# Kernel optimization log

Measured on AMD Instinct MI355X. Metric: run time of the kernel, lower is better.

Reference implementation:

```python
import jax, jax.numpy as jnp
import numpy as np

INPUT, HIDDEN, OUTPUT = 512, 1024, 512

def setup_inputs() -> dict:
    key = jax.random.key(0)
    ks = jax.random.split(key, 7)
    s_in = 1.0 / np.sqrt(INPUT)
    s_h = 1.0 / np.sqrt(HIDDEN)
    return {
        "x": jax.random.normal(ks[0], (64, 512, INPUT), dtype=jnp.float32),
        "W_in": jax.random.uniform(ks[1], (INPUT, HIDDEN), minval=-s_in, maxval=s_in, dtype=jnp.float32),
        "b_in": jax.random.uniform(ks[2], (HIDDEN,), minval=-s_in, maxval=s_in, dtype=jnp.float32),
        "W_h": jax.random.uniform(ks[3], (HIDDEN, HIDDEN), minval=-s_h, maxval=s_h, dtype=jnp.float32),
        "b_h": jax.random.uniform(ks[4], (HIDDEN,), minval=-s_h, maxval=s_h, dtype=jnp.float32),
        "W_out": jax.random.uniform(ks[5], (HIDDEN, OUTPUT), minval=-s_h, maxval=s_h, dtype=jnp.float32),
        "b_out": jax.random.uniform(ks[6], (OUTPUT,), minval=-s_h, maxval=s_h, dtype=jnp.float32),
    }

def reference(x, W_in, b_in, W_h, b_h, W_out, b_out):
    B = x.shape[0]
    # Precompute input projection for all timesteps: [B, T, H]
    xin = jnp.einsum('bti,ih->bth', x, W_in) + b_in
    h0 = jnp.zeros((B, W_h.shape[0]), dtype=x.dtype)

    def step(h, xin_t):
        h_new = jnp.tanh(xin_t + h @ W_h + b_h)
        return h_new, None

    h_final, _ = jax.lax.scan(step, h0, jnp.swapaxes(xin, 0, 1))  # scan over T
    return h_final @ W_out + b_out
```

## Files before the change

### kernel.cpp

```cpp
#include <hip/hip_runtime.h>


typedef float f32x4 __attribute__((ext_vector_type(4)));
typedef short bf16x8 __attribute__((ext_vector_type(8)));
typedef short s16x4 __attribute__((ext_vector_type(4)));
typedef unsigned u32;
typedef unsigned u32x2 __attribute__((ext_vector_type(2)));
typedef unsigned u32x4 __attribute__((ext_vector_type(4)));

__device__ __forceinline__ short f2bf(float f) {
  unsigned u = __builtin_bit_cast(unsigned, f);
  u = (u + 0x7FFFu + ((u >> 16) & 1u)) >> 16;
  return (short)u;
}
__device__ __forceinline__ float bf2f(short s) {
  unsigned u = ((unsigned)(unsigned short)s) << 16;
  return __builtin_bit_cast(float, u);
}

__global__ __launch_bounds__(256) void k_prep(const float* __restrict__ Wh,
                                              short* __restrict__ wprep) {
  const int wgid = blockIdx.x;
  const int cj = wgid >> 2, wslot = wgid & 3;
  const int tid = threadIdx.x, lane = tid & 63, sub = tid >> 6;
  const int l15 = lane & 15, lhi = lane >> 4;
  #pragma unroll
  for (int ktl = 0; ktl < 2; ++ktl) {
    int kt = sub * 2 + ktl;
    #pragma unroll
    for (int nt = 0; nt < 4; ++nt) {
      const float* src = Wh + (size_t)(wslot * 256 + kt * 32 + lhi * 8) * 1024
                            + cj * 64 + nt * 16 + l15;
      bf16x8 v;
      #pragma unroll
      for (int j = 0; j < 8; ++j) v[j] = f2bf(src[(size_t)j * 1024]);
      *(bf16x8*)(wprep + ((((size_t)(cj * 4 + wslot) * 8 + kt) * 4 + nt) * 64 + lane) * 8) = v;
    }
  }
}

__global__ __launch_bounds__(256) void k_inproj(const float* __restrict__ X,
                                                const float* __restrict__ Win,
                                                const float* __restrict__ bin,
                                                short* __restrict__ xin) {
  __shared__ __align__(16) short Al[128][40];
  __shared__ __align__(16) short Bl[128][40];
  __shared__ __align__(16) short Cl[128][64];
  const int m0g = blockIdx.x * 128, n0g = blockIdx.y * 128;
  const int tid = threadIdx.x;
  const int lane = tid & 63, wave = tid >> 6;
  const int wm = (wave & 1) * 64, wn = (wave >> 1) * 64;
  const int l15 = lane & 15, lhi = lane >> 4;

  f32x4 acc[4][4] = {};

  for (int kb = 0; kb < 512; kb += 32) {
    #pragma unroll
    for (int i = 0; i < 4; ++i) {
      int flat = tid + i * 256;
      int row = flat >> 3, k4 = (flat & 7) * 4;
      float4 v = *(const float4*)(X + (size_t)(m0g + row) * 512 + kb + k4);
      s16x4 s; s[0] = f2bf(v.x); s[1] = f2bf(v.y); s[2] = f2bf(v.z); s[3] = f2bf(v.w);
      *(s16x4*)&Al[row][k4] = s;
    }
    #pragma unroll
    for (int i = 0; i < 4; ++i) {
      int flat = tid + i * 256;
      int n = flat & 127, k0 = (flat >> 7) * 4;
      const float* wp = Win + (size_t)(kb + k0) * 1024 + n0g + n;
      s16x4 s;
      s[0] = f2bf(wp[0]); s[1] = f2bf(wp[1024]); s[2] = f2bf(wp[2048]); s[3] = f2bf(wp[3072]);
      *(s16x4*)&Bl[n][k0] = s;
    }
    __syncthreads();
    bf16x8 a[4], b[4];
    #pragma unroll
    for (int mt = 0; mt < 4; ++mt) a[mt] = *(const bf16x8*)&Al[wm + mt * 16 + l15][lhi * 8];
    #pragma unroll
    for (int nt = 0; nt < 4; ++nt) b[nt] = *(const bf16x8*)&Bl[wn + nt * 16 + l15][lhi * 8];
    #pragma unroll
    for (int mt = 0; mt < 4; ++mt)
      #pragma unroll
      for (int nt = 0; nt < 4; ++nt)
        acc[mt][nt] = __builtin_amdgcn_mfma_f32_16x16x32_bf16(a[mt], b[nt], acc[mt][nt], 0, 0, 0);
    __syncthreads();
  }

  float bias[4];
  #pragma unroll
  for (int nt = 0; nt < 4; ++nt) bias[nt] = bin[n0g + wn + nt * 16 + l15];

  const size_t gbase = ((size_t)(m0g >> 13) * 512 + (m0g & 511)) * 16 + ((m0g >> 9) & 15);
  #pragma unroll
  for (int h = 0; h < 2; ++h) {
    if ((wave >> 1) == h) {
      #pragma unroll
      for (int mt = 0; mt < 4; ++mt)
        #pragma unroll
        for (int nt = 0; nt < 4; ++nt)
          #pragma unroll
          for (int r = 0; r < 4; ++r) {
            int row = wm + mt * 16 + lhi * 4 + r;
            Cl[row][nt * 16 + l15] = f2bf(acc[mt][nt][r] + bias[nt]);
          }
    }
    __syncthreads();
    {
      int row = tid >> 1, c0 = (tid & 1) * 32;
      const int4* src = (const int4*)&Cl[row][c0];
      int4* dst = (int4*)(xin + (gbase + (size_t)row * 16) * 1024 + n0g + h * 64 + c0);
      dst[0] = src[0]; dst[1] = src[1]; dst[2] = src[2]; dst[3] = src[3];
    }
    __syncthreads();
  }
}

__global__ __launch_bounds__(256, 1) void k_recur(const short* __restrict__ xin,
                                                  const short* __restrict__ wprep,
                                                  const float* __restrict__ bh,
                                                  short* __restrict__ hfrag,
                                                  u32* __restrict__ flags,
                                                  float* __restrict__ hfin) {
  const int wg = blockIdx.x;
  const int g = wg & 3, cj = wg >> 2;
  const int tid = threadIdx.x, lane = tid & 63, wave = tid >> 6;
  const int l15 = lane & 15, lhi = lane >> 4;
  const int colbase = cj << 6, rowbase = g << 4;
  __shared__ __align__(16) float part[4][16][68];

  bf16x8 wf[8][4];
  {
    const short* wb = wprep + ((size_t)(cj * 4 + wave) << 14) + lane * 8;
    #pragma unroll
    for (int kt = 0; kt < 8; ++kt)
      #pragma unroll
      for (int nt = 0; nt < 4; ++nt) {
        u32x4 r;
        const short* ap = wb + ((kt * 4 + nt) << 9);
        asm volatile("global_load_dwordx4 %0, %1, off" : "=v"(r) : "v"(ap) : "memory");
        wf[kt][nt] = __builtin_bit_cast(bf16x8, r);
      }
    asm volatile("s_waitcnt vmcnt(0)" ::: "memory");
    __builtin_amdgcn_sched_barrier(0);
  }

  const int erow = tid >> 4, ec0 = (tid & 15) << 2;
  const int n0 = colbase + ec0;
  const float4 bh4 = *(const float4*)(bh + n0);
  const short* xbase = xin + (size_t)g * 512 * 16384 + erow * 1024 + n0;
  const u32* fp = flags + (g << 4) + (wave << 2) + (lane & 3);
  u32* myflag = flags + (g << 4) + cj;
  const short* hrd0 = hfrag + ((g << 2) + wave) * 4096 + lane * 8;
  const short* hrd1 = hrd0 + 2048;
  short* hwr = hfrag + (g << 14) + ((n0 >> 8) << 12) + (((n0 >> 5) & 7) << 9)
                     + ((((n0 & 31) >> 3) << 4) + erow) * 8 + (n0 & 7);

  {
    s16x4 xs = *(const s16x4*)xbase;
    float h0 = tanhf(bh4.x + bf2f(xs[0]));
    float h1 = tanhf(bh4.y + bf2f(xs[1]));
    float h2 = tanhf(bh4.z + bf2f(xs[2]));
    float h3 = tanhf(bh4.w + bf2f(xs[3]));
    u32x2 wv;
    wv[0] = ((u32)(unsigned short)f2bf(h1) << 16) | (unsigned short)f2bf(h0);
    wv[1] = ((u32)(unsigned short)f2bf(h3) << 16) | (unsigned short)f2bf(h2);
    short* dst = hwr + 65536;
    asm volatile("global_store_dwordx2 %0, %1, off sc1" :: "v"(dst), "v"(wv) : "memory");
    asm volatile("s_waitcnt vmcnt(0)" ::: "memory");
    __syncthreads();
    if (tid == 0) {
      u32 fv = 1;
      asm volatile("global_store_dword %0, %1, off sc1" :: "v"(myflag), "v"(fv) : "memory");
    }
  }

  for (int t = 1; t < 512; ++t) {
    s16x4 xs = *(const s16x4*)(xbase + (size_t)t * 16384);
    for (;;) {
      u32 f;
      asm volatile("global_load_dword %0, %1, off sc1\n\ts_waitcnt vmcnt(0)"
                   : "=v"(f) : "v"(fp) : "memory");
      __builtin_amdgcn_sched_barrier(0);
      if (__all((int)(f >= (u32)t))) break;
    }
    const int poff = (t & 1) << 16;
    const short* hs0 = hrd0 + poff;
    const short* hs1 = hrd1 + poff;
    u32x4 ar[8];
    #pragma unroll
    for (int kt = 0; kt < 4; ++kt) {
      asm volatile("global_load_dwordx4 %0, %1, off offset:%c2 sc1"
                   : "=v"(ar[kt]) : "v"(hs0), "i"(kt * 1024) : "memory");
      asm volatile("global_load_dwordx4 %0, %1, off offset:%c2 sc1"
                   : "=v"(ar[kt + 4]) : "v"(hs1), "i"(kt * 1024) : "memory");
    }
    asm volatile("s_waitcnt vmcnt(0)" ::: "memory");
    __builtin_amdgcn_sched_barrier(0);

    f32x4 acc[4] = {};
    #pragma unroll
    for (int kt = 0; kt < 8; ++kt) {
      bf16x8 a = __builtin_bit_cast(bf16x8, ar[kt]);
      #pragma unroll
      for (int nt = 0; nt < 4; ++nt)
        acc[nt] = __builtin_amdgcn_mfma_f32_16x16x32_bf16(a, wf[kt][nt], acc[nt], 0, 0, 0);
    }
    #pragma unroll
    for (int nt = 0; nt < 4; ++nt)
      #pragma unroll
      for (int r = 0; r < 4; ++r)
        part[wave][lhi * 4 + r][nt * 16 + l15] = acc[nt][r];
    __syncthreads();

    f32x4 p0 = *(const f32x4*)&part[0][erow][ec0];
    f32x4 p1 = *(const f32x4*)&part[1][erow][ec0];
    f32x4 p2 = *(const f32x4*)&part[2][erow][ec0];
    f32x4 p3 = *(const f32x4*)&part[3][erow][ec0];
    f32x4 ps = (p0 + p1) + (p2 + p3);
    float h0 = tanhf(ps[0] + bh4.x + bf2f(xs[0]));
    float h1 = tanhf(ps[1] + bh4.y + bf2f(xs[1]));
    float h2 = tanhf(ps[2] + bh4.z + bf2f(xs[2]));
    float h3 = tanhf(ps[3] + bh4.w + bf2f(xs[3]));

    if (t < 511) {
      u32x2 wv;
      wv[0] = ((u32)(unsigned short)f2bf(h1) << 16) | (unsigned short)f2bf(h0);
      wv[1] = ((u32)(unsigned short)f2bf(h3) << 16) | (unsigned short)f2bf(h2);
      short* dst = hwr + (((t + 1) & 1) << 16);
      asm volatile("global_store_dwordx2 %0, %1, off sc1" :: "v"(dst), "v"(wv) : "memory");
      asm volatile("s_waitcnt vmcnt(0)" ::: "memory");
      __syncthreads();
      if (tid == 0) {
        u32 fv = (u32)(t + 1);
        asm volatile("global_store_dword %0, %1, off sc1" :: "v"(myflag), "v"(fv) : "memory");
      }
    } else {
      float4 hf4; hf4.x = h0; hf4.y = h1; hf4.z = h2; hf4.w = h3;
      *(float4*)(hfin + (rowbase + erow) * 1024 + n0) = hf4;
      __syncthreads();
    }
  }
}

__global__ __launch_bounds__(256) void k_out(const float* __restrict__ hfin,
                                             const float* __restrict__ Wout,
                                             const float* __restrict__ bout,
                                             float* __restrict__ out) {
  __shared__ __align__(16) float hrow[1024];
  const int b = blockIdx.x >> 1;
  const int c0 = (blockIdx.x & 1) << 8;
  const int tid = threadIdx.x;
  #pragma unroll
  for (int i = 0; i < 4; ++i) hrow[tid + i * 256] = hfin[b * 1024 + tid + i * 256];
  __syncthreads();
  const int col = c0 + tid;
  const float* wp = Wout + col;
  float a0 = bout[col], a1 = 0, a2 = 0, a3 = 0, a4 = 0, a5 = 0, a6 = 0, a7 = 0;
  #pragma unroll 4
  for (int k = 0; k < 1024; k += 8) {
    a0 += hrow[k + 0] * wp[(size_t)(k + 0) * 512];
    a1 += hrow[k + 1] * wp[(size_t)(k + 1) * 512];
    a2 += hrow[k + 2] * wp[(size_t)(k + 2) * 512];
    a3 += hrow[k + 3] * wp[(size_t)(k + 3) * 512];
    a4 += hrow[k + 4] * wp[(size_t)(k + 4) * 512];
    a5 += hrow[k + 5] * wp[(size_t)(k + 5) * 512];
    a6 += hrow[k + 6] * wp[(size_t)(k + 6) * 512];
    a7 += hrow[k + 7] * wp[(size_t)(k + 7) * 512];
  }
  out[b * 512 + col] = ((a0 + a1) + (a2 + a3)) + ((a4 + a5) + (a6 + a7));
}

extern "C" void kernel_launch(void* const* d_in, const int* in_sizes, int n_in,
                              void* d_out, int out_size, void* d_ws, size_t ws_size,
                              hipStream_t stream) {
  const float* x    = (const float*)d_in[0];
  const float* Win  = (const float*)d_in[1];
  const float* bin  = (const float*)d_in[2];
  const float* Wh   = (const float*)d_in[3];
  const float* bh   = (const float*)d_in[4];
  const float* Wout = (const float*)d_in[5];
  const float* bout = (const float*)d_in[6];

  char* ws = (char*)d_ws;
  short* xin   = (short*)ws;
  short* wprep = (short*)(ws + 67108864);
  short* hfrag = (short*)(ws + 69206016);
  u32*   flags = (u32*)(ws + 69468160);
  float* hfin  = (float*)(ws + 69469184);

  hipMemsetAsync(flags, 0, 1024, stream);
  hipLaunchKernelGGL(k_prep, dim3(64), dim3(256), 0, stream, Wh, wprep);
  hipLaunchKernelGGL(k_inproj, dim3(256, 8), dim3(256), 0, stream, x, Win, bin, xin);
  hipLaunchKernelGGL(k_recur, dim3(64), dim3(256), 0, stream,
                     xin, wprep, bh, hfrag, flags, hfin);
  hipLaunchKernelGGL(k_out, dim3(128), dim3(256), 0, stream, hfin, Wout, bout, (float*)d_out);
}
```

Before: 1.431 ms.

## Stage h fragments through LDS and publish per-wave flags instead of per-block

Each workgroup now writes its new hidden-state fragment into shared memory first and then stores it to global memory as contiguous per-thread chunks, so the writes are coalesced. Readiness is signalled with one flag per wave instead of one per workgroup, and consumers poll 16 flags per wave. This drops the post-store __syncthreads before signalling, shortening the critical path of each serial timestep. It adds an LDS round trip and barrier, and the flag array grows by four times.

```diff
diff --git a/kernel.cpp b/kernel.cpp
--- a/kernel.cpp
+++ b/kernel.cpp
@@ -127,6 +127,7 @@
   const int l15 = lane & 15, lhi = lane >> 4;
   const int colbase = cj << 6, rowbase = g << 4;
   __shared__ __align__(16) float part[4][16][68];
+  __shared__ __align__(16) short hshare[1024];
 
   bf16x8 wf[8][4];
   {
@@ -148,12 +149,12 @@
   const int n0 = colbase + ec0;
   const float4 bh4 = *(const float4*)(bh + n0);
   const short* xbase = xin + (size_t)g * 512 * 16384 + erow * 1024 + n0;
-  const u32* fp = flags + (g << 4) + (wave << 2) + (lane & 3);
-  u32* myflag = flags + (g << 4) + cj;
+  const u32* fp = flags + (g << 6) + (wave << 4) + (lane & 15);
+  u32* myflag = flags + (g << 6) + (cj << 2) + wave;
   const short* hrd0 = hfrag + ((g << 2) + wave) * 4096 + lane * 8;
   const short* hrd1 = hrd0 + 2048;
-  short* hwr = hfrag + (g << 14) + ((n0 >> 8) << 12) + (((n0 >> 5) & 7) << 9)
-                     + ((((n0 & 31) >> 3) << 4) + erow) * 8 + (n0 & 7);
+  const int lds_off = ((ec0 >> 5) << 9) + ((((ec0 >> 3) & 3) << 4) + erow) * 8 + (ec0 & 7);
+  short* gst = hfrag + (((((g << 2) + (cj >> 2)) << 3) + ((cj & 3) << 1)) << 9) + tid * 4;
 
   {
     s16x4 xs = *(const s16x4*)xbase;
@@ -161,14 +162,14 @@
     float h1 = tanhf(bh4.y + bf2f(xs[1]));
     float h2 = tanhf(bh4.z + bf2f(xs[2]));
     float h3 = tanhf(bh4.w + bf2f(xs[3]));
-    u32x2 wv;
-    wv[0] = ((u32)(unsigned short)f2bf(h1) << 16) | (unsigned short)f2bf(h0);
-    wv[1] = ((u32)(unsigned short)f2bf(h3) << 16) | (unsigned short)f2bf(h2);
-    short* dst = hwr + 65536;
-    asm volatile("global_store_dwordx2 %0, %1, off sc1" :: "v"(dst), "v"(wv) : "memory");
+    s16x4 hv; hv[0] = f2bf(h0); hv[1] = f2bf(h1); hv[2] = f2bf(h2); hv[3] = f2bf(h3);
+    *(s16x4*)&hshare[lds_off] = hv;
+    __syncthreads();
+    u32x2 sv = *(const u32x2*)&hshare[tid * 4];
+    short* dst = gst + 65536;
+    asm volatile("global_store_dwordx2 %0, %1, off sc1" :: "v"(dst), "v"(sv) : "memory");
     asm volatile("s_waitcnt vmcnt(0)" ::: "memory");
-    __syncthreads();
-    if (tid == 0) {
+    if ((tid & 63) == 0) {
       u32 fv = 1;
       asm volatile("global_store_dword %0, %1, off sc1" :: "v"(myflag), "v"(fv) : "memory");
     }
@@ -208,8 +209,8 @@
     #pragma unroll
     for (int nt = 0; nt < 4; ++nt)
       #pragma unroll
-      for (int r = 0; r < 4; ++r)
-        part[wave][lhi * 4 + r][nt * 16 + l15] = acc[nt][r];
+      for (int rr = 0; rr < 4; ++rr)
+        part[wave][lhi * 4 + rr][nt * 16 + l15] = acc[nt][rr];
     __syncthreads();
 
     f32x4 p0 = *(const f32x4*)&part[0][erow][ec0];
@@ -223,21 +224,20 @@
     float h3 = tanhf(ps[3] + bh4.w + bf2f(xs[3]));
 
     if (t < 511) {
-      u32x2 wv;
-      wv[0] = ((u32)(unsigned short)f2bf(h1) << 16) | (unsigned short)f2bf(h0);
-      wv[1] = ((u32)(unsigned short)f2bf(h3) << 16) | (unsigned short)f2bf(h2);
-      short* dst = hwr + (((t + 1) & 1) << 16);
-      asm volatile("global_store_dwordx2 %0, %1, off sc1" :: "v"(dst), "v"(wv) : "memory");
+      s16x4 hv; hv[0] = f2bf(h0); hv[1] = f2bf(h1); hv[2] = f2bf(h2); hv[3] = f2bf(h3);
+      *(s16x4*)&hshare[lds_off] = hv;
+      __syncthreads();
+      u32x2 sv = *(const u32x2*)&hshare[tid * 4];
+      short* dst = gst + (((t + 1) & 1) << 16);
+      asm volatile("global_store_dwordx2 %0, %1, off sc1" :: "v"(dst), "v"(sv) : "memory");
       asm volatile("s_waitcnt vmcnt(0)" ::: "memory");
-      __syncthreads();
-      if (tid == 0) {
+      if ((tid & 63) == 0) {
         u32 fv = (u32)(t + 1);
         asm volatile("global_store_dword %0, %1, off sc1" :: "v"(myflag), "v"(fv) : "memory");
       }
     } else {
       float4 hf4; hf4.x = h0; hf4.y = h1; hf4.z = h2; hf4.w = h3;
       *(float4*)(hfin + (rowbase + erow) * 1024 + n0) = hf4;
-      __syncthreads();
     }
   }
 }
```

New measurement: 1.989 ms. 1.39x slower.

## Use per-wave completion flags, pipelined flag polling and double-buffered partial sums

Applied to the files above, without the earlier changes.

The recurrence kernel now publishes one flag per wave instead of one per workgroup. This removes the block-wide barrier before each flag store, since each wave signals once its own rows of h are written. Flag polling keeps several loads in flight at once, and the x-projection load is issued as asynchronous inline asm. The LDS partial-sum buffer is double-buffered by timestep parity so the trailing barrier can be dropped. The flag array grows fourfold, which the host allocation must cover, and there are more flag reads per step.

```diff
diff --git a/kernel.cpp b/kernel.cpp
--- a/kernel.cpp
+++ b/kernel.cpp
@@ -126,7 +126,7 @@
   const int tid = threadIdx.x, lane = tid & 63, wave = tid >> 6;
   const int l15 = lane & 15, lhi = lane >> 4;
   const int colbase = cj << 6, rowbase = g << 4;
-  __shared__ __align__(16) float part[4][16][68];
+  __shared__ __align__(16) float part[2][4][16][68];
 
   bf16x8 wf[8][4];
   {
@@ -148,12 +148,13 @@
   const int n0 = colbase + ec0;
   const float4 bh4 = *(const float4*)(bh + n0);
   const short* xbase = xin + (size_t)g * 512 * 16384 + erow * 1024 + n0;
-  const u32* fp = flags + (g << 4) + (wave << 2) + (lane & 3);
-  u32* myflag = flags + (g << 4) + cj;
+  const u32* fp = flags + (g << 6) + (wave << 4) + (lane & 15);
+  u32* myflag = flags + (g << 6) + (cj << 2) + wave;
   const short* hrd0 = hfrag + ((g << 2) + wave) * 4096 + lane * 8;
   const short* hrd1 = hrd0 + 2048;
-  short* hwr = hfrag + (g << 14) + ((n0 >> 8) << 12) + (((n0 >> 5) & 7) << 9)
-                     + ((((n0 & 31) >> 3) << 4) + erow) * 8 + (n0 & 7);
+  const int wk = n0 >> 8, ktp = (n0 >> 5) & 7, e = n0 & 31;
+  const int plane = ((e >> 3) << 4) | erow, pj = n0 & 7;
+  short* hwr = hfrag + (((((g << 2) + wk) << 3) + ktp) << 9) + (plane << 3) + pj;
 
   {
     s16x4 xs = *(const s16x4*)xbase;
@@ -167,21 +168,38 @@
     short* dst = hwr + 65536;
     asm volatile("global_store_dwordx2 %0, %1, off sc1" :: "v"(dst), "v"(wv) : "memory");
     asm volatile("s_waitcnt vmcnt(0)" ::: "memory");
-    __syncthreads();
-    if (tid == 0) {
+    __builtin_amdgcn_sched_barrier(0);
+    if (lane == 0) {
       u32 fv = 1;
       asm volatile("global_store_dword %0, %1, off sc1" :: "v"(myflag), "v"(fv) : "memory");
     }
   }
 
+#define POLL_STAGE(fr)                                                      \
+  asm volatile("s_waitcnt vmcnt(3)" ::: "memory");                          \
+  __builtin_amdgcn_sched_barrier(0);                                        \
+  if (__all((int)(fr >= tt))) break;                                        \
+  asm volatile("global_load_dword %0, %1, off sc1" : "=v"(fr) : "v"(fp) : "memory");
+
   for (int t = 1; t < 512; ++t) {
-    s16x4 xs = *(const s16x4*)(xbase + (size_t)t * 16384);
+    const u32 tt = (u32)t;
+    u32x2 xsr;
+    {
+      const short* xa = xbase + (size_t)t * 16384;
+      asm volatile("global_load_dwordx2 %0, %1, off" : "=v"(xsr) : "v"(xa) : "memory");
+    }
+    u32 f0, f1, f2, f3;
+    asm volatile("global_load_dword %0, %1, off sc1" : "=v"(f0) : "v"(fp) : "memory");
+    asm volatile("global_load_dword %0, %1, off sc1" : "=v"(f1) : "v"(fp) : "memory");
+    asm volatile("global_load_dword %0, %1, off sc1" : "=v"(f2) : "v"(fp) : "memory");
+    asm volatile("global_load_dword %0, %1, off sc1" : "=v"(f3) : "v"(fp) : "memory");
+    asm volatile("s_waitcnt vmcnt(4)" ::: "memory");
+    __builtin_amdgcn_sched_barrier(0);
     for (;;) {
-      u32 f;
-      asm volatile("global_load_dword %0, %1, off sc1\n\ts_waitcnt vmcnt(0)"
-                   : "=v"(f) : "v"(fp) : "memory");
-      __builtin_amdgcn_sched_barrier(0);
-      if (__all((int)(f >= (u32)t))) break;
+      POLL_STAGE(f0)
+      POLL_STAGE(f1)
+      POLL_STAGE(f2)
+      POLL_STAGE(f3)
     }
     const int poff = (t & 1) << 16;
     const short* hs0 = hrd0 + poff;
@@ -205,18 +223,20 @@
       for (int nt = 0; nt < 4; ++nt)
         acc[nt] = __builtin_amdgcn_mfma_f32_16x16x32_bf16(a, wf[kt][nt], acc[nt], 0, 0, 0);
     }
+    const int p = t & 1;
     #pragma unroll
     for (int nt = 0; nt < 4; ++nt)
       #pragma unroll
-      for (int r = 0; r < 4; ++r)
-        part[wave][lhi * 4 + r][nt * 16 + l15] = acc[nt][r];
-    __syncthreads();
-
-    f32x4 p0 = *(const f32x4*)&part[0][erow][ec0];
-    f32x4 p1 = *(const f32x4*)&part[1][erow][ec0];
-    f32x4 p2 = *(const f32x4*)&part[2][erow][ec0];
-    f32x4 p3 = *(const f32x4*)&part[3][erow][ec0];
+      for (int rr = 0; rr < 4; ++rr)
+        part[p][wave][lhi * 4 + rr][nt * 16 + l15] = acc[nt][rr];
+    __syncthreads();
+
+    f32x4 p0 = *(const f32x4*)&part[p][0][erow][ec0];
+    f32x4 p1 = *(const f32x4*)&part[p][1][erow][ec0];
+    f32x4 p2 = *(const f32x4*)&part[p][2][erow][ec0];
+    f32x4 p3 = *(const f32x4*)&part[p][3][erow][ec0];
     f32x4 ps = (p0 + p1) + (p2 + p3);
+    s16x4 xs = __builtin_bit_cast(s16x4, xsr);
     float h0 = tanhf(ps[0] + bh4.x + bf2f(xs[0]));
     float h1 = tanhf(ps[1] + bh4.y + bf2f(xs[1]));
     float h2 = tanhf(ps[2] + bh4.z + bf2f(xs[2]));
@@ -229,17 +249,17 @@
       short* dst = hwr + (((t + 1) & 1) << 16);
       asm volatile("global_store_dwordx2 %0, %1, off sc1" :: "v"(dst), "v"(wv) : "memory");
       asm volatile("s_waitcnt vmcnt(0)" ::: "memory");
-      __syncthreads();
-      if (tid == 0) {
+      __builtin_amdgcn_sched_barrier(0);
+      if (lane == 0) {
         u32 fv = (u32)(t + 1);
         asm volatile("global_store_dword %0, %1, off sc1" :: "v"(myflag), "v"(fv) : "memory");
       }
     } else {
       float4 hf4; hf4.x = h0; hf4.y = h1; hf4.z = h2; hf4.w = h3;
       *(float4*)(hfin + (rowbase + erow) * 1024 + n0) = hf4;
-      __syncthreads();
-    }
-  }
+    }
+  }
+#undef POLL_STAGE
 }
 
 __global__ __launch_bounds__(256) void k_out(const float* __restrict__ hfin,
```

After: 2.421 ms. 1.69x slower.
